# Optimization experiments

Measured on AMD Instinct MI355X. Metric: run time of the kernel, lower is better.

The kernel has to match this reference:

```python
import jax, jax.numpy as jnp
import numpy as np

H = 2048
Q_RANK = 256
SCALE = float(np.sqrt(Q_RANK))


def setup_inputs() -> dict:
    key = jax.random.key(0)
    k_x, k_s, k_a, k_o, k_b = jax.random.split(key, 5)
    B, L = 4, 4096
    x = jax.random.normal(k_x, (B, L, H), dtype=jnp.float32)
    # nn.Linear(H, q_rank, bias=False): weight [q_rank, H]; y = x @ W.T -> store transposed [H, q_rank]
    Ws = jax.random.normal(k_s, (H, Q_RANK), dtype=jnp.float32) / np.sqrt(H)
    Wa = jax.random.normal(k_a, (H, Q_RANK), dtype=jnp.float32) / np.sqrt(H)
    Wo = jax.random.normal(k_o, (H, H), dtype=jnp.float32) / np.sqrt(H)
    bo = jax.random.normal(k_b, (H,), dtype=jnp.float32) * 0.01
    return {"x": x, "Ws": Ws, "Wa": Wa, "Wo": Wo, "bo": bo}


def reference(x, Ws, Wa, Wo, bo):
    # x: [B, L, H]
    B, L, _ = x.shape
    state = jnp.einsum('blh,hr->blr', x, Ws)   # [B, L, r]
    action = jnp.einsum('blh,hr->blr', x, Wa)  # [B, L, r]
    q_values = jnp.einsum('bir,bjr->bij', state, action) / SCALE  # [B, L, L]
    # causal mask: position i attends to j <= i
    causal = jnp.tril(jnp.ones((L, L), dtype=bool))
    q_values = jnp.where(causal, q_values, -jnp.inf)
    weights = jax.nn.softmax(q_values, axis=-1)  # [B, L, L]
    out = jnp.einsum('bij,bjh->bih', weights, x)  # weights @ x (x acts as V)
    return jnp.einsum('bih,ho->bio', out, Wo.T) + bo  # out_proj: y = out @ Wo_lin.T; Wo stored as [H,H] input-major
```

## Files before the change

kernel.cpp:

```cpp
#include <hip/hip_runtime.h>
#include <hip/hip_bf16.h>
#include <cstdint>
#include <cstddef>
#include <cmath>

typedef __bf16 bf16_t;
typedef __bf16 bf16x8 __attribute__((ext_vector_type(8)));
typedef __bf16 bf16x4v __attribute__((ext_vector_type(4)));
typedef float f32x4 __attribute__((ext_vector_type(4)));

#define B_SZ 4
#define L_SZ 4096
#define H_SZ 2048
#define R_SZ 256
#define EXP_SC 0.090168440f
#define E2_ELEMS 8912896L
#define E2_BYTES 17825792L

#define GLDS16(gaddr, laddr)                                                    \
  __builtin_amdgcn_global_load_lds(                                             \
      (const __attribute__((address_space(1))) void*)(gaddr),                   \
      (__attribute__((address_space(3))) void*)(laddr), 16, 0, 0)

__device__ __forceinline__ f32x4 mfma16(bf16x8 a, bf16x8 b, f32x4 c) {
  return __builtin_amdgcn_mfma_f32_16x16x32_bf16(a, b, c, 0, 0, 0);
}

__device__ __forceinline__ float rsum16(float v) {
  v += __shfl_xor(v, 1, 16);
  v += __shfl_xor(v, 2, 16);
  v += __shfl_xor(v, 4, 16);
  v += __shfl_xor(v, 8, 16);
  return v;
}

__global__ void conv_kernel(const float* __restrict__ x, const float* __restrict__ Ws,
                            const float* __restrict__ Wa, const float* __restrict__ Wo,
                            bf16_t* __restrict__ xb, bf16_t* __restrict__ Wst,
                            bf16_t* __restrict__ Wat, bf16_t* __restrict__ Wob,
                            float* __restrict__ lsum) {
  const int tid = blockIdx.x * blockDim.x + threadIdx.x;
  const int stride = gridDim.x * blockDim.x;
  const int n4 = B_SZ * L_SZ * H_SZ / 4;
  for (int i = tid; i < n4; i += stride) {
    float4 v = reinterpret_cast<const float4*>(x)[i];
    bf16x4v o;
    o[0] = (bf16_t)v.x; o[1] = (bf16_t)v.y; o[2] = (bf16_t)v.z; o[3] = (bf16_t)v.w;
    reinterpret_cast<bf16x4v*>(xb)[i] = o;
  }
  for (int idx = tid; idx < R_SZ * H_SZ; idx += stride) {
    const int rr = idx >> 11;
    const int h  = idx & (H_SZ - 1);
    Wst[idx] = (bf16_t)Ws[h * R_SZ + rr];
    Wat[idx] = (bf16_t)Wa[h * R_SZ + rr];
  }
  for (int idx = tid; idx < H_SZ * H_SZ; idx += stride) {
    Wob[idx] = (bf16_t)Wo[idx];
  }
  for (int idx = tid; idx < B_SZ * L_SZ; idx += stride) lsum[idx] = 0.0f;
}


#define G8_STG(P, REGION, BUFOFF, HALF)                                        \
  GLDS16((P)[0], lds + (REGION) + (BUFOFF) + (HALF)*16384 + ldst0);            \
  GLDS16((P)[1], lds + (REGION) + (BUFOFF) + (HALF)*16384 + ldst1);            \
  (P)[0] += 128; (P)[1] += 128;

#define G8_LDA(MH, BO) {                                                       \
  const char* ap_ = lds + (BO) + (MH)*16384;                                   \
  fa[0][0] = *(const bf16x8*)(ap_ + aOff0);                                    \
  fa[0][1] = *(const bf16x8*)(ap_ + aOff1);                                    \
  fa[1][0] = *(const bf16x8*)(ap_ + 4096 + aOff0);                             \
  fa[1][1] = *(const bf16x8*)(ap_ + 4096 + aOff1);                             \
  fa[2][0] = *(const bf16x8*)(ap_ + 8192 + aOff0);                             \
  fa[2][1] = *(const bf16x8*)(ap_ + 8192 + aOff1);                             \
  fa[3][0] = *(const bf16x8*)(ap_ + 12288 + aOff0);                            \
  fa[3][1] = *(const bf16x8*)(ap_ + 12288 + aOff1); }

#define G8_LDB(NH, BO) {                                                       \
  const char* bp_ = lds + 65536 + (BO) + (NH)*16384;                           \
  fb[NH][0][0] = *(const bf16x8*)(bp_ + bOff0);                                \
  fb[NH][0][1] = *(const bf16x8*)(bp_ + bOff1);                                \
  fb[NH][1][0] = *(const bf16x8*)(bp_ + 8192 + bOff0);                         \
  fb[NH][1][1] = *(const bf16x8*)(bp_ + 8192 + bOff1); }

#define G8_MM1(AM, AN, MF, NH, J)                                              \
  acc[AM][AN] = mfma16(fa[MF][1], fb[NH][J][1],                                \
                 mfma16(fa[MF][0], fb[NH][J][0], acc[AM][AN]))

#define G8_MM(MH, NH)                                                          \
  G8_MM1((MH)*4+0, (NH)*2+0, 0, NH, 0); G8_MM1((MH)*4+0, (NH)*2+1, 0, NH, 1); \
  G8_MM1((MH)*4+1, (NH)*2+0, 1, NH, 0); G8_MM1((MH)*4+1, (NH)*2+1, 1, NH, 1); \
  G8_MM1((MH)*4+2, (NH)*2+0, 2, NH, 0); G8_MM1((MH)*4+2, (NH)*2+1, 2, NH, 1); \
  G8_MM1((MH)*4+3, (NH)*2+0, 3, NH, 0); G8_MM1((MH)*4+3, (NH)*2+1, 3, NH, 1)

#define G8_PHASE(LOADS, STAGES, WAITS, MH, NH)                                 \
  LOADS;                                                                       \
  STAGES;                                                                      \
  __builtin_amdgcn_sched_barrier(0);                                           \
  __builtin_amdgcn_s_barrier();                                                \
  __builtin_amdgcn_s_setprio(1);                                               \
  G8_MM(MH, NH);                                                               \
  __builtin_amdgcn_s_setprio(0);                                               \
  WAITS;                                                                       \
  __builtin_amdgcn_sched_barrier(0);                                           \
  __builtin_amdgcn_s_barrier();

__device__ __forceinline__ void gemm8_core(
    const char* Ag, const char* Bg, long aRowB, long bRowB, int NT,
    char* lds, f32x4 (&acc)[8][4])
{
  const int t = threadIdx.x;
  const int l = t & 63;
  const int wid = t >> 6;
  const int wr = wid >> 2;
  const int wc = wid & 3;
  const int l15 = l & 15;
  const int l4 = l >> 4;
  const int swzm = (l15 & 7) << 4;
  const int aOff0 = (wr * 16 + l15) * 128 + ((l4 * 16) ^ swzm);
  const int aOff1 = (wr * 16 + l15) * 128 + ((64 + l4 * 16) ^ swzm);
  const int bOff0 = (wc * 16 + l15) * 128 + ((l4 * 16) ^ swzm);
  const int bOff1 = (wc * 16 + l15) * 128 + ((64 + l4 * 16) ^ swzm);
  const int d0 = t * 16, d1 = t * 16 + 8192;
  const int r0 = d0 >> 7, r1 = d1 >> 7;
  const int s0 = (d0 & 127) ^ ((r0 & 7) << 4);
  const int s1 = (d1 & 127) ^ ((r1 & 7) << 4);
  const char* pA0[2] = { Ag + (long)r0 * aRowB + s0, Ag + (long)r1 * aRowB + s1 };
  const char* pA1[2] = { Ag + (long)(128 + r0) * aRowB + s0, Ag + (long)(128 + r1) * aRowB + s1 };
  const char* pB0[2] = { Bg + (long)r0 * bRowB + s0, Bg + (long)r1 * bRowB + s1 };
  const char* pB1[2] = { Bg + (long)(128 + r0) * bRowB + s0, Bg + (long)(128 + r1) * bRowB + s1 };
  const int ldst0 = wid * 1024, ldst1 = wid * 1024 + 8192;
  bf16x8 fa[4][2], fb[2][2][2];

  G8_STG(pA0, 0, 0, 0);
  G8_STG(pB0, 65536, 0, 0);
  G8_STG(pA1, 0, 0, 1);
  G8_STG(pB1, 65536, 0, 1);
  G8_STG(pA0, 0, 32768, 0);
  G8_STG(pB0, 65536, 32768, 0);
  asm volatile("s_waitcnt vmcnt(4)" ::: "memory");
  __builtin_amdgcn_sched_barrier(0);
  __builtin_amdgcn_s_barrier();

  int bufOff = 0;
  for (int T = 0; T < NT - 2; ++T) {
    const int ob = bufOff ^ 32768;
    G8_PHASE(G8_LDA(0, bufOff) G8_LDB(0, bufOff), G8_STG(pA1, 0, ob, 1), , 0, 0);
    G8_PHASE(G8_LDB(1, bufOff), G8_STG(pB1, 65536, ob, 1), , 0, 1);
    G8_PHASE(G8_LDA(1, bufOff), G8_STG(pA0, 0, bufOff, 0), , 1, 0);
    G8_PHASE(, G8_STG(pB0, 65536, bufOff, 0),
             asm volatile("s_waitcnt vmcnt(4)" ::: "memory"), 1, 1);
    bufOff ^= 32768;
  }
  {
    const int ob = bufOff ^ 32768;
    G8_PHASE(G8_LDA(0, bufOff) G8_LDB(0, bufOff), G8_STG(pA1, 0, ob, 1), , 0, 0);
    G8_PHASE(G8_LDB(1, bufOff), G8_STG(pB1, 65536, ob, 1), , 0, 1);
    G8_PHASE(G8_LDA(1, bufOff), , , 1, 0);
    G8_PHASE(, , asm volatile("s_waitcnt vmcnt(0)" ::: "memory"), 1, 1);
    bufOff ^= 32768;
  }
  {
    G8_PHASE(G8_LDA(0, bufOff) G8_LDB(0, bufOff), , , 0, 0);
    G8_PHASE(G8_LDB(1, bufOff), , , 0, 1);
    G8_PHASE(G8_LDA(1, bufOff), , , 1, 0);
    G8_PHASE(, , , 1, 1);
  }
}

__global__ __launch_bounds__(512) void vq8_kernel(
    const bf16_t* __restrict__ Wob, const bf16_t* __restrict__ xb, bf16_t* __restrict__ VT,
    const bf16_t* __restrict__ Wst, const bf16_t* __restrict__ Wat,
    bf16_t* __restrict__ Qb, bf16_t* __restrict__ Kb)
{
  extern __shared__ char lds[];
  const int f = blockIdx.x;
  const int t = threadIdx.x, l = t & 63, wid = t >> 6;
  const int wr = wid >> 2, wc = wid & 3, l15 = l & 15, l4 = l >> 4;
  if (f < 128) {
    const int proj = f >> 6;
    const long mBase = (long)(f & 63) * 256;
    const bf16_t* W = proj ? Wat : Wst;
    bf16_t* Cp = proj ? Kb : Qb;
    f32x4 acc[8][4] = {};
    gemm8_core((const char*)xb + mBase * (H_SZ * 2), (const char*)W,
               H_SZ * 2, H_SZ * 2, H_SZ / 64, lds, acc);
#pragma unroll
    for (int am = 0; am < 8; ++am) {
#pragma unroll
      for (int an = 0; an < 4; ++an) {
        const long row = mBase + wr * 16 + am * 32 + l4 * 4;
        const int col = wc * 16 + an * 64 + l15;
#pragma unroll
        for (int r = 0; r < 4; ++r)
          Cp[(row + r) * R_SZ + col] = (bf16_t)acc[am][an][r];
      }
    }
  } else {
    const int g = f - 128;
    const int lg = (g & 7) * 64 + (g >> 3);
    const int xo = lg & 7;
    const int yj = (lg >> 3) & 15;
    const int b  = lg >> 7;
    const long mBase = (long)xo * 256;
    const long nBase = (long)yj * 256;
    f32x4 acc[8][4] = {};
    gemm8_core((const char*)Wob + mBase * (H_SZ * 2),
               (const char*)xb + ((long)b * L_SZ + nBase) * (H_SZ * 2),
               H_SZ * 2, H_SZ * 2, H_SZ / 64, lds, acc);
    bf16_t* Cp = VT + (long)b * H_SZ * L_SZ;
#pragma unroll
    for (int am = 0; am < 8; ++am) {
#pragma unroll
      for (int an = 0; an < 4; ++an) {
        const long row = mBase + wr * 16 + am * 32 + l4 * 4;
        const long col = nBase + wc * 16 + an * 64 + l15;
#pragma unroll
        for (int r = 0; r < 4; ++r)
          Cp[(row + r) * L_SZ + col] = (bf16_t)acc[am][an][r];
      }
    }
  }
}

__global__ __launch_bounds__(512) void ep8_kernel(
    const bf16_t* __restrict__ Qb, const bf16_t* __restrict__ Kb,
    bf16_t* __restrict__ E, float* __restrict__ lsum)
{
  extern __shared__ char lds[];
  const int f = blockIdx.x;
  const int lg = (f & 7) * 68 + (f >> 3);
  const int b = lg / 136;
  const int t136 = lg - b * 136;
  int P = (int)((sqrtf((float)(8 * t136 + 1)) - 1.0f) * 0.5f);
  while ((P + 1) * (P + 2) / 2 <= t136) ++P;
  while (P * (P + 1) / 2 > t136) --P;
  const int Jp = t136 - P * (P + 1) / 2;

  f32x4 acc[8][4] = {};
  gemm8_core((const char*)Qb + ((long)b * L_SZ + P * 256) * (R_SZ * 2),
             (const char*)Kb + ((long)b * L_SZ + Jp * 256) * (R_SZ * 2),
             R_SZ * 2, R_SZ * 2, R_SZ / 64, lds, acc);
  const int t = threadIdx.x, l = t & 63, wid = t >> 6;
  const int wr = wid >> 2, wc = wid & 3, l15 = l & 15, l4 = l >> 4;
  bf16_t* Ep = E + (long)b * E2_ELEMS + 32768L * P * (P + 1);
  const long ldaE = (long)(P + 1) * 256;
  float* lp = lsum + (long)b * L_SZ + P * 256;
  const bool diag = (Jp == P);
#pragma unroll
  for (int am = 0; am < 8; ++am) {
    const int rowi = wr * 16 + am * 32 + l4 * 4;
#pragma unroll
    for (int r = 0; r < 4; ++r) {
      float s = 0.0f;
#pragma unroll
      for (int an = 0; an < 4; ++an) {
        const int coli = wc * 16 + an * 64 + l15;
        float p = exp2f(acc[am][an][r] * EXP_SC);
        if (diag && coli > rowi + r) p = 0.0f;
        Ep[(long)(rowi + r) * ldaE + Jp * 256 + coli] = (bf16_t)p;
        s += p;
      }
      s = rsum16(s);
      if (l15 == 0) atomicAdd(lp + rowi + r, s);
    }
  }
}

__global__ __launch_bounds__(512) void pv8_kernel(
    const bf16_t* __restrict__ E, const bf16_t* __restrict__ VT,
    const float* __restrict__ lsum, const float* __restrict__ bo,
    float* __restrict__ out)
{
  extern __shared__ char lds[];
  const int f = blockIdx.x;
  const int lg = (f & 7) * 32 + (f >> 3);
  const int yj = lg & 7;
  const int pr = (lg >> 3) & 7;
  const int b  = lg >> 6;
  const int nBase = yj * 256;
  const int t = threadIdx.x, l = t & 63, wid = t >> 6;
  const int wr = wid >> 2, wc = wid & 3, l15 = l & 15, l4 = l >> 4;

#pragma unroll
  for (int s = 0; s < 2; ++s) {
    const int mt = s ? pr : (15 - pr);
    f32x4 acc[8][4] = {};
    const char* Ag = (const char*)E + (long)b * E2_BYTES + 65536L * mt * (mt + 1);
    const char* Bg = (const char*)VT + ((long)b * H_SZ + nBase) * (L_SZ * 2);
    gemm8_core(Ag, Bg, (long)(mt + 1) * 512, L_SZ * 2, (mt + 1) * 4, lds, acc);
#pragma unroll
    for (int am = 0; am < 8; ++am) {
      const long rowG = (long)b * L_SZ + mt * 256 + wr * 16 + am * 32 + l4 * 4;
      float linv[4];
#pragma unroll
      for (int r = 0; r < 4; ++r) linv[r] = 1.0f / lsum[rowG + r];
#pragma unroll
      for (int an = 0; an < 4; ++an) {
        const int col = nBase + wc * 16 + an * 64 + l15;
        const float bias = bo[col];
#pragma unroll
        for (int r = 0; r < 4; ++r)
          out[(rowG + r) * H_SZ + col] = acc[am][an][r] * linv[r] + bias;
      }
    }
  }
}

extern "C" void kernel_launch(void* const* d_in, const int* in_sizes, int n_in,
                              void* d_out, int out_size, void* d_ws, size_t ws_size,
                              hipStream_t stream) {
  const float* x  = (const float*)d_in[0];
  const float* Ws = (const float*)d_in[1];
  const float* Wa = (const float*)d_in[2];
  const float* Wo = (const float*)d_in[3];
  const float* bo = (const float*)d_in[4];
  float* out = (float*)d_out;

  char* ws = (char*)d_ws;
  bf16_t* xb  = (bf16_t*)(ws + 0);
  bf16_t* Wst = (bf16_t*)(ws + 67108864);
  bf16_t* Wat = (bf16_t*)(ws + 68157440);
  bf16_t* Wob = (bf16_t*)(ws + 69206016);
  bf16_t* Qb  = (bf16_t*)(ws + 77594624);
  bf16_t* Kb  = (bf16_t*)(ws + 85983232);
  bf16_t* VT  = (bf16_t*)(ws + 94371840);
  float*  lsum = (float*)(ws + 161480704);
  bf16_t* E   = (bf16_t*)(ws + 0);

  hipFuncSetAttribute((const void*)vq8_kernel, hipFuncAttributeMaxDynamicSharedMemorySize, 131072);
  hipFuncSetAttribute((const void*)ep8_kernel, hipFuncAttributeMaxDynamicSharedMemorySize, 131072);
  hipFuncSetAttribute((const void*)pv8_kernel, hipFuncAttributeMaxDynamicSharedMemorySize, 131072);

  conv_kernel<<<dim3(2048), dim3(256), 0, stream>>>(x, Ws, Wa, Wo, xb, Wst, Wat, Wob, lsum);
  vq8_kernel<<<dim3(640), dim3(512), 131072, stream>>>(Wob, xb, VT, Wst, Wat, Qb, Kb);
  ep8_kernel<<<dim3(544), dim3(512), 131072, stream>>>(Qb, Kb, E, lsum);
  pv8_kernel<<<dim3(256), dim3(512), 131072, stream>>>(E, VT, lsum, bo, out);
}
```

Baseline: 383.9 us.

## Merge four GEMM phases into two barrier regions with LDS prefetch overlap

Restructures the main GEMM loop from four barrier-separated phases into two regions per K-tile. Each region issues more global-to-LDS stages and LDS fragment loads before a larger MFMA block, and the second A fragment load is prefetched behind the first block's MFMAs with explicit lgkmcnt waits. This halves the number of workgroup barriers per tile and overlaps LDS reads with compute. In exchange it raises register pressure from holding more fragments at once and depends on the hand-placed waitcnt values being correct.

```diff
diff --git a/kernel.cpp b/kernel.cpp
--- a/kernel.cpp
+++ b/kernel.cpp
@@ -94,14 +94,27 @@
   G8_MM1((MH)*4+2, (NH)*2+0, 2, NH, 0); G8_MM1((MH)*4+2, (NH)*2+1, 2, NH, 1); \
   G8_MM1((MH)*4+3, (NH)*2+0, 3, NH, 0); G8_MM1((MH)*4+3, (NH)*2+1, 3, NH, 1)
 
-#define G8_PHASE(LOADS, STAGES, WAITS, MH, NH)                                 \
-  LOADS;                                                                       \
-  STAGES;                                                                      \
+#define G8_REGION1(BO, S1A, S1B)                                               \
+  G8_LDA(0, BO);                                                               \
+  G8_LDB(0, BO);                                                               \
+  G8_LDB(1, BO);                                                               \
+  S1A; S1B;                                                                    \
+  __builtin_amdgcn_s_setprio(1);                                               \
+  G8_MM(0, 0);                                                                 \
+  G8_MM(0, 1);                                                                 \
+  __builtin_amdgcn_s_setprio(0);                                               \
+  G8_LDA(1, BO);                                                               \
+  asm volatile("s_waitcnt lgkmcnt(8)" ::: "memory");                           \
   __builtin_amdgcn_sched_barrier(0);                                           \
-  __builtin_amdgcn_s_barrier();                                                \
+  __builtin_amdgcn_s_barrier();
+
+#define G8_REGION2(S2A, S2B, WAITS)                                            \
+  S2A; S2B;                                                                    \
   __builtin_amdgcn_s_setprio(1);                                               \
-  G8_MM(MH, NH);                                                               \
+  G8_MM(1, 0);                                                                 \
+  G8_MM(1, 1);                                                                 \
   __builtin_amdgcn_s_setprio(0);                                               \
+  asm volatile("s_waitcnt lgkmcnt(0)" ::: "memory");                           \
   WAITS;                                                                       \
   __builtin_amdgcn_sched_barrier(0);                                           \
   __builtin_amdgcn_s_barrier();
@@ -146,26 +159,20 @@
   int bufOff = 0;
   for (int T = 0; T < NT - 2; ++T) {
     const int ob = bufOff ^ 32768;
-    G8_PHASE(G8_LDA(0, bufOff) G8_LDB(0, bufOff), G8_STG(pA1, 0, ob, 1), , 0, 0);
-    G8_PHASE(G8_LDB(1, bufOff), G8_STG(pB1, 65536, ob, 1), , 0, 1);
-    G8_PHASE(G8_LDA(1, bufOff), G8_STG(pA0, 0, bufOff, 0), , 1, 0);
-    G8_PHASE(, G8_STG(pB0, 65536, bufOff, 0),
-             asm volatile("s_waitcnt vmcnt(4)" ::: "memory"), 1, 1);
+    G8_REGION1(bufOff, G8_STG(pA1, 0, ob, 1), G8_STG(pB1, 65536, ob, 1));
+    G8_REGION2(G8_STG(pA0, 0, bufOff, 0), G8_STG(pB0, 65536, bufOff, 0),
+               asm volatile("s_waitcnt vmcnt(4)" ::: "memory"));
     bufOff ^= 32768;
   }
   {
     const int ob = bufOff ^ 32768;
-    G8_PHASE(G8_LDA(0, bufOff) G8_LDB(0, bufOff), G8_STG(pA1, 0, ob, 1), , 0, 0);
-    G8_PHASE(G8_LDB(1, bufOff), G8_STG(pB1, 65536, ob, 1), , 0, 1);
-    G8_PHASE(G8_LDA(1, bufOff), , , 1, 0);
-    G8_PHASE(, , asm volatile("s_waitcnt vmcnt(0)" ::: "memory"), 1, 1);
+    G8_REGION1(bufOff, G8_STG(pA1, 0, ob, 1), G8_STG(pB1, 65536, ob, 1));
+    G8_REGION2(, , asm volatile("s_waitcnt vmcnt(0)" ::: "memory"));
     bufOff ^= 32768;
   }
   {
-    G8_PHASE(G8_LDA(0, bufOff) G8_LDB(0, bufOff), , , 0, 0);
-    G8_PHASE(G8_LDB(1, bufOff), , , 0, 1);
-    G8_PHASE(G8_LDA(1, bufOff), , , 1, 0);
-    G8_PHASE(, , , 1, 1);
+    G8_REGION1(bufOff, , );
+    G8_REGION2(, , );
   }
 }
 
```

New measurement: 374.3 us. 2.5% less time.

## Restructure GEMM main loop into two barrier phases and split Q/K projection tiles

Applied to the files above, without the earlier changes.

The shared GEMM core drops from four barrier-separated phases per K-step to two, using lgkmcnt waits and conditional staging in a single loop instead of peeled tail iterations. A FULLN template parameter lets the Q/K projection use 256x128 tiles. This doubles the projection block count (768 total blocks) and puts the V projection blocks first. The Wo bf16 conversion is vectorized to float4 loads. Together these aim to cut barrier overhead and improve load balance, at the risk of less latency hiding per phase and a changed ordering of LDS reads and staging writes.

```diff
diff --git a/kernel.cpp b/kernel.cpp
--- a/kernel.cpp
+++ b/kernel.cpp
@@ -54,8 +54,11 @@
     Wst[idx] = (bf16_t)Ws[h * R_SZ + rr];
     Wat[idx] = (bf16_t)Wa[h * R_SZ + rr];
   }
-  for (int idx = tid; idx < H_SZ * H_SZ; idx += stride) {
-    Wob[idx] = (bf16_t)Wo[idx];
+  for (int idx = tid; idx < H_SZ * H_SZ / 4; idx += stride) {
+    float4 v = reinterpret_cast<const float4*>(Wo)[idx];
+    bf16x4v o;
+    o[0] = (bf16_t)v.x; o[1] = (bf16_t)v.y; o[2] = (bf16_t)v.z; o[3] = (bf16_t)v.w;
+    reinterpret_cast<bf16x4v*>(Wob)[idx] = o;
   }
   for (int idx = tid; idx < B_SZ * L_SZ; idx += stride) lsum[idx] = 0.0f;
 }
@@ -94,18 +97,7 @@
   G8_MM1((MH)*4+2, (NH)*2+0, 2, NH, 0); G8_MM1((MH)*4+2, (NH)*2+1, 2, NH, 1); \
   G8_MM1((MH)*4+3, (NH)*2+0, 3, NH, 0); G8_MM1((MH)*4+3, (NH)*2+1, 3, NH, 1)
 
-#define G8_PHASE(LOADS, STAGES, WAITS, MH, NH)                                 \
-  LOADS;                                                                       \
-  STAGES;                                                                      \
-  __builtin_amdgcn_sched_barrier(0);                                           \
-  __builtin_amdgcn_s_barrier();                                                \
-  __builtin_amdgcn_s_setprio(1);                                               \
-  G8_MM(MH, NH);                                                               \
-  __builtin_amdgcn_s_setprio(0);                                               \
-  WAITS;                                                                       \
-  __builtin_amdgcn_sched_barrier(0);                                           \
-  __builtin_amdgcn_s_barrier();
-
+template <bool FULLN>
 __device__ __forceinline__ void gemm8_core(
     const char* Ag, const char* Bg, long aRowB, long bRowB, int NT,
     char* lds, f32x4 (&acc)[8][4])
@@ -136,7 +128,7 @@
   G8_STG(pA0, 0, 0, 0);
   G8_STG(pB0, 65536, 0, 0);
   G8_STG(pA1, 0, 0, 1);
-  G8_STG(pB1, 65536, 0, 1);
+  if constexpr (FULLN) { G8_STG(pB1, 65536, 0, 1); }
   G8_STG(pA0, 0, 32768, 0);
   G8_STG(pB0, 65536, 32768, 0);
   asm volatile("s_waitcnt vmcnt(4)" ::: "memory");
@@ -144,28 +136,42 @@
   __builtin_amdgcn_s_barrier();
 
   int bufOff = 0;
-  for (int T = 0; T < NT - 2; ++T) {
+  for (int T = 0; T < NT; ++T) {
     const int ob = bufOff ^ 32768;
-    G8_PHASE(G8_LDA(0, bufOff) G8_LDB(0, bufOff), G8_STG(pA1, 0, ob, 1), , 0, 0);
-    G8_PHASE(G8_LDB(1, bufOff), G8_STG(pB1, 65536, ob, 1), , 0, 1);
-    G8_PHASE(G8_LDA(1, bufOff), G8_STG(pA0, 0, bufOff, 0), , 1, 0);
-    G8_PHASE(, G8_STG(pB0, 65536, bufOff, 0),
-             asm volatile("s_waitcnt vmcnt(4)" ::: "memory"), 1, 1);
+    const bool stg1 = (T < NT - 1);
+    const bool stg2 = (T < NT - 2);
+    G8_LDA(0, bufOff);
+    G8_LDB(0, bufOff);
+    if constexpr (FULLN) { G8_LDB(1, bufOff); }
+    if (stg1) {
+      G8_STG(pA1, 0, ob, 1);
+      if constexpr (FULLN) { G8_STG(pB1, 65536, ob, 1); }
+    }
+    __builtin_amdgcn_s_setprio(1);
+    G8_MM(0, 0);
+    if constexpr (FULLN) { G8_MM(0, 1); }
+    __builtin_amdgcn_s_setprio(0);
+    G8_LDA(1, bufOff);
+    asm volatile("s_waitcnt lgkmcnt(8)" ::: "memory");
+    __builtin_amdgcn_sched_barrier(0);
+    __builtin_amdgcn_s_barrier();
+    if (stg2) {
+      G8_STG(pA0, 0, bufOff, 0);
+      G8_STG(pB0, 65536, bufOff, 0);
+    }
+    __builtin_amdgcn_s_setprio(1);
+    G8_MM(1, 0);
+    if constexpr (FULLN) { G8_MM(1, 1); }
+    __builtin_amdgcn_s_setprio(0);
+    asm volatile("s_waitcnt lgkmcnt(0)" ::: "memory");
+    if (stg2) {
+      asm volatile("s_waitcnt vmcnt(4)" ::: "memory");
+    } else if (stg1) {
+      asm volatile("s_waitcnt vmcnt(0)" ::: "memory");
+    }
+    __builtin_amdgcn_sched_barrier(0);
+    __builtin_amdgcn_s_barrier();
     bufOff ^= 32768;
-  }
-  {
-    const int ob = bufOff ^ 32768;
-    G8_PHASE(G8_LDA(0, bufOff) G8_LDB(0, bufOff), G8_STG(pA1, 0, ob, 1), , 0, 0);
-    G8_PHASE(G8_LDB(1, bufOff), G8_STG(pB1, 65536, ob, 1), , 0, 1);
-    G8_PHASE(G8_LDA(1, bufOff), , , 1, 0);
-    G8_PHASE(, , asm volatile("s_waitcnt vmcnt(0)" ::: "memory"), 1, 1);
-    bufOff ^= 32768;
-  }
-  {
-    G8_PHASE(G8_LDA(0, bufOff) G8_LDB(0, bufOff), , , 0, 0);
-    G8_PHASE(G8_LDB(1, bufOff), , , 0, 1);
-    G8_PHASE(G8_LDA(1, bufOff), , , 1, 0);
-    G8_PHASE(, , , 1, 1);
   }
 }
 
@@ -178,37 +184,17 @@
   const int f = blockIdx.x;
   const int t = threadIdx.x, l = t & 63, wid = t >> 6;
   const int wr = wid >> 2, wc = wid & 3, l15 = l & 15, l4 = l >> 4;
-  if (f < 128) {
-    const int proj = f >> 6;
-    const long mBase = (long)(f & 63) * 256;
-    const bf16_t* W = proj ? Wat : Wst;
-    bf16_t* Cp = proj ? Kb : Qb;
-    f32x4 acc[8][4] = {};
-    gemm8_core((const char*)xb + mBase * (H_SZ * 2), (const char*)W,
-               H_SZ * 2, H_SZ * 2, H_SZ / 64, lds, acc);
-#pragma unroll
-    for (int am = 0; am < 8; ++am) {
-#pragma unroll
-      for (int an = 0; an < 4; ++an) {
-        const long row = mBase + wr * 16 + am * 32 + l4 * 4;
-        const int col = wc * 16 + an * 64 + l15;
-#pragma unroll
-        for (int r = 0; r < 4; ++r)
-          Cp[(row + r) * R_SZ + col] = (bf16_t)acc[am][an][r];
-      }
-    }
-  } else {
-    const int g = f - 128;
-    const int lg = (g & 7) * 64 + (g >> 3);
+  f32x4 acc[8][4] = {};
+  if (f < 512) {
+    const int lg = (f & 7) * 64 + (f >> 3);
     const int xo = lg & 7;
     const int yj = (lg >> 3) & 15;
     const int b  = lg >> 7;
     const long mBase = (long)xo * 256;
     const long nBase = (long)yj * 256;
-    f32x4 acc[8][4] = {};
-    gemm8_core((const char*)Wob + mBase * (H_SZ * 2),
-               (const char*)xb + ((long)b * L_SZ + nBase) * (H_SZ * 2),
-               H_SZ * 2, H_SZ * 2, H_SZ / 64, lds, acc);
+    gemm8_core<true>((const char*)Wob + mBase * (H_SZ * 2),
+                     (const char*)xb + ((long)b * L_SZ + nBase) * (H_SZ * 2),
+                     H_SZ * 2, H_SZ * 2, H_SZ / 64, lds, acc);
     bf16_t* Cp = VT + (long)b * H_SZ * L_SZ;
 #pragma unroll
     for (int am = 0; am < 8; ++am) {
@@ -219,6 +205,30 @@
 #pragma unroll
         for (int r = 0; r < 4; ++r)
           Cp[(row + r) * L_SZ + col] = (bf16_t)acc[am][an][r];
+      }
+    }
+  } else {
+    const int qf = f - 512;
+    const int lg = (qf & 7) * 32 + (qf >> 3);
+    const int m = lg & 63;
+    const int n = (lg >> 6) & 1;
+    const int proj = lg >> 7;
+    const long mBase = (long)m * 256;
+    const long nBase = (long)n * 128;
+    const bf16_t* W = proj ? Wat : Wst;
+    bf16_t* Cp = proj ? Kb : Qb;
+    gemm8_core<false>((const char*)xb + mBase * (H_SZ * 2),
+                      (const char*)W + nBase * (H_SZ * 2),
+                      H_SZ * 2, H_SZ * 2, H_SZ / 64, lds, acc);
+#pragma unroll
+    for (int am = 0; am < 8; ++am) {
+#pragma unroll
+      for (int an = 0; an < 2; ++an) {
+        const long row = mBase + wr * 16 + am * 32 + l4 * 4;
+        const long col = nBase + wc * 16 + an * 64 + l15;
+#pragma unroll
+        for (int r = 0; r < 4; ++r)
+          Cp[(row + r) * R_SZ + col] = (bf16_t)acc[am][an][r];
       }
     }
   }
@@ -239,9 +249,9 @@
   const int Jp = t136 - P * (P + 1) / 2;
 
   f32x4 acc[8][4] = {};
-  gemm8_core((const char*)Qb + ((long)b * L_SZ + P * 256) * (R_SZ * 2),
-             (const char*)Kb + ((long)b * L_SZ + Jp * 256) * (R_SZ * 2),
-             R_SZ * 2, R_SZ * 2, R_SZ / 64, lds, acc);
+  gemm8_core<true>((const char*)Qb + ((long)b * L_SZ + P * 256) * (R_SZ * 2),
+                   (const char*)Kb + ((long)b * L_SZ + Jp * 256) * (R_SZ * 2),
+                   R_SZ * 2, R_SZ * 2, R_SZ / 64, lds, acc);
   const int t = threadIdx.x, l = t & 63, wid = t >> 6;
   const int wr = wid >> 2, wc = wid & 3, l15 = l & 15, l4 = l >> 4;
   bf16_t* Ep = E + (long)b * E2_ELEMS + 32768L * P * (P + 1);
@@ -289,7 +299,7 @@
     f32x4 acc[8][4] = {};
     const char* Ag = (const char*)E + (long)b * E2_BYTES + 65536L * mt * (mt + 1);
     const char* Bg = (const char*)VT + ((long)b * H_SZ + nBase) * (L_SZ * 2);
-    gemm8_core(Ag, Bg, (long)(mt + 1) * 512, L_SZ * 2, (mt + 1) * 4, lds, acc);
+    gemm8_core<true>(Ag, Bg, (long)(mt + 1) * 512, L_SZ * 2, (mt + 1) * 4, lds, acc);
 #pragma unroll
     for (int am = 0; am < 8; ++am) {
       const long rowG = (long)b * L_SZ + mt * 256 + wr * 16 + am * 32 + l4 * 4;
@@ -334,7 +344,7 @@
   hipFuncSetAttribute((const void*)pv8_kernel, hipFuncAttributeMaxDynamicSharedMemorySize, 131072);
 
   conv_kernel<<<dim3(2048), dim3(256), 0, stream>>>(x, Ws, Wa, Wo, xb, Wst, Wat, Wob, lsum);
-  vq8_kernel<<<dim3(640), dim3(512), 131072, stream>>>(Wob, xb, VT, Wst, Wat, Qb, Kb);
+  vq8_kernel<<<dim3(768), dim3(512), 131072, stream>>>(Wob, xb, VT, Wst, Wat, Qb, Kb);
   ep8_kernel<<<dim3(544), dim3(512), 131072, stream>>>(Qb, Kb, E, lsum);
   pv8_kernel<<<dim3(256), dim3(512), 131072, stream>>>(E, VT, lsum, bo, out);
 }
```

After: 371.8 us. 3.2% less time.
